# Kernel tuning notes

Hardware: AMD Instinct MI355X
Metric: run time of the kernel (lower is better)

## Reference

```python
import jax, jax.numpy as jnp
import numpy as np

B, L, N_KERNELS = 16, 4096, 512
KSS = [7, 9, 11]


def _make_params():
    """Replicates ROCKET.__init__ random kernel generation (numpy RNG, seed 0).

    Note: the torch code builds Conv1d with padding=2*padding (padding doubled),
    computes the padding from the *float* dilation, and casts dilation to int
    for the conv. We reproduce that exactly.
    """
    rng = np.random.default_rng(0)
    ks_a, d_a, pad_a, w_l, b_l = [], [], [], [], []
    for _ in range(N_KERNELS):
        ks = int(rng.choice(KSS))
        d_f = 2.0 ** rng.uniform(0.0, np.log2((L - 1) // (ks - 1)))
        d = int(d_f)
        p0 = int((ks - 1) * d_f // 2) if rng.integers(2) == 1 else 0
        pad = 2 * p0  # conv1d padding arg is 2*padding in the source
        w = rng.standard_normal(ks).astype(np.float32)
        w -= w.mean()  # weight -= weight.mean() (c_in=1 -> mean over ks)
        b = np.float32(2.0 * (rng.random() - 0.5))
        ks_a.append(ks); d_a.append(d); pad_a.append(pad)
        w_l.append(w); b_l.append(b)
    P = max(pad_a)  # global pad applied once to x; per-kernel offset corrects
    groups = {}
    order = []
    for ks in KSS:
        ids = [i for i in range(N_KERNELS) if ks_a[i] == ks]
        order += ids
        off = np.stack([[P - pad_a[i] + k * d_a[i] for k in range(ks)] for i in ids]).astype(np.int32)
        lout = np.array([L + 2 * pad_a[i] - d_a[i] * (ks - 1) for i in ids], np.int32)
        w = np.stack([w_l[i] for i in ids]).astype(np.float32)
        b = np.array([b_l[i] for i in ids], np.float32)
        groups[ks] = (w, b, off, lout)
    perm = np.argsort(np.array(order)).astype(np.int32)  # grouped -> original order
    return groups, perm, P


def setup_inputs() -> dict:
    key = jax.random.key(0)
    x = jax.random.normal(key, (B, 1, L), dtype=jnp.float32)
    groups, perm, P = _make_params()
    inp = {"x": x, "perm": jnp.asarray(perm), "P": int(P)}
    for gi, ks in enumerate(KSS):
        w, b, off, lout = groups[ks]
        inp[f"w{gi}"] = jnp.asarray(w)
        inp[f"b{gi}"] = jnp.asarray(b)
        inp[f"off{gi}"] = jnp.asarray(off)
        inp[f"lout{gi}"] = jnp.asarray(lout)
    return inp


def _group_feats(x_pad, w, b, off, lout, Lmax, Lp):
    # x_pad: [B, Lp]; w: [G, ks]; off: [G, ks]; lout: [G]
    t = jnp.arange(Lmax)
    out = b[None, :, None]  # [1, G, 1]
    ks = w.shape[-1]
    for k in range(ks):  # ks <= 11 taps of the dilated conv, batched over G kernels
        idx = jnp.clip(off[:, k][:, None] + t[None, :], 0, Lp - 1)  # [G, Lmax]
        out = out + w[:, k][None, :, None] * x_pad[:, idx]  # [B, G, Lmax]
    valid = (t[None, :] < lout[:, None])[None]  # [1, G, Lmax]
    mx = jnp.max(jnp.where(valid, out, jnp.finfo(out.dtype).min), axis=-1)  # [B, G]
    ppv = jnp.where(valid, out > 0, False).sum(-1).astype(out.dtype) / lout[None, :].astype(out.dtype)
    return mx, ppv


def reference(x, w0, b0, off0, lout0, w1, b1, off1, lout1, w2, b2, off2, lout2, perm, P):
    xs = x[:, 0, :]  # c_in = 1
    Lseq = xs.shape[-1]
    Lmax = 2 * Lseq + 16  # static bound: lout <= 2L + max(ks)
    Lp = Lseq + 2 * P
    x_pad = jnp.pad(xs, ((0, 0), (P, P)))
    mxs, ppvs = [], []
    for (w, b, off, lout) in ((w0, b0, off0, lout0), (w1, b1, off1, lout1), (w2, b2, off2, lout2)):
        mx, ppv = _group_feats(x_pad, w, b, off, lout, Lmax, Lp)
        mxs.append(mx)
        ppvs.append(ppv)
    mx = jnp.concatenate(mxs, axis=1)[:, perm]   # [B, n_kernels] original order
    ppv = jnp.concatenate(ppvs, axis=1)[:, perm]
    # torch.cat interleaves (max_i, ppv_i) along feature dim
    return jnp.stack([mx, ppv], axis=2).reshape(x.shape[0], -1)
```

## Files before the change

### kernel.cpp

```cpp
#include <hip/hip_runtime.h>
#include <math.h>

#define LSEQ 4096
#define NK 512
#define NB 16
#define NT 1024
#define CK 16
#define NCH (NK / CK)

typedef float v2f __attribute__((ext_vector_type(2)));

template <int KS>
__device__ __forceinline__ void rocket_body(
    const float* __restrict__ sx,
    const float* __restrict__ w, const float* __restrict__ bias,
    const int* __restrict__ off, const int* __restrict__ lout,
    int P, int li,
    float* smxc, int* scntc, int* sLoc)
{
    const int tid = threadIdx.x;

    float wk[KS];
#pragma unroll
    for (int k = 0; k < KS; ++k) wk[k] = w[li * KS + k];
    const int o0  = off[li * KS + 0];
    const int o1  = off[li * KS + 1];
    const int d   = o1 - o0;
    const int pad = P - o0;
    const float bi = bias[li];
    const int   Lo = lout[li];

    int t_lo = min(pad, Lo);
    int t_hi = min(Lo, LSEQ - (KS - 1) * d + pad);
    if (t_hi < t_lo) t_hi = t_lo;
    int T0 = (t_lo + 3) & ~3;
    int T1 = t_hi & ~3;
    if (T1 < T0) { T0 = 0; T1 = 0; }

    float mx  = -INFINITY;
    int   cnt = 0;

    for (int t = tid; t < T0; t += NT) {
        float y = bi;
        int idx = t - pad;
#pragma unroll
        for (int k = 0; k < KS; ++k) {
            int ic = min(max(idx, 0), LSEQ - 1);
            float xv = sx[ic];
            xv = ((unsigned)idx < (unsigned)LSEQ) ? xv : 0.0f;
            y = fmaf(wk[k], xv, y);
            idx += d;
        }
        mx = fmaxf(mx, y); cnt += (y > 0.0f);
    }

    int ebk[KS];
#pragma unroll
    for (int k = 0; k < KS; ++k) {
        const int A0 = T0 - pad + k * d;
        const int rk = A0 & 3;
        ebk[k] = rk * LSEQ + (k * d - pad - rk);
    }
    v2f mx2 = { -INFINITY, -INFINITY };
    for (int t = T0 + 4 * tid; t < T1; t += 4 * NT) {
        v2f y01 = { bi, bi }, y23 = { bi, bi };
#pragma unroll
        for (int kb = 0; kb < KS; kb += 4) {
            const int ke = (kb + 4 < KS) ? (kb + 4) : KS;
            float4 Xc[4];
#pragma unroll
            for (int k = kb; k < ke; ++k)
                Xc[k - kb] = *(const float4*)(sx + (t + ebk[k]));
#pragma unroll
            for (int k = kb; k < ke; ++k) {
                const v2f wv  = { wk[k], wk[k] };
                const v2f xlo = { Xc[k - kb].x, Xc[k - kb].y };
                const v2f xhi = { Xc[k - kb].z, Xc[k - kb].w };
                y01 = __builtin_elementwise_fma(wv, xlo, y01);
                y23 = __builtin_elementwise_fma(wv, xhi, y23);
            }
        }
        mx2 = __builtin_elementwise_max(mx2, __builtin_elementwise_max(y01, y23));
        cnt += (y01.x > 0.0f);
        cnt += (y01.y > 0.0f);
        cnt += (y23.x > 0.0f);
        cnt += (y23.y > 0.0f);
    }
    mx = fmaxf(mx, fmaxf(mx2.x, mx2.y));

    for (int t = T1 + tid; t < Lo; t += NT) {
        float y = bi;
        int idx = t - pad;
#pragma unroll
        for (int k = 0; k < KS; ++k) {
            int ic = min(max(idx, 0), LSEQ - 1);
            float xv = sx[ic];
            xv = ((unsigned)idx < (unsigned)LSEQ) ? xv : 0.0f;
            y = fmaf(wk[k], xv, y);
            idx += d;
        }
        mx = fmaxf(mx, y); cnt += (y > 0.0f);
    }

#pragma unroll
    for (int o = 32; o > 0; o >>= 1) {
        mx = fmaxf(mx, __shfl_down(mx, o, 64));
        cnt += __shfl_down(cnt, o, 64);
    }
    const int wid = tid >> 6;
    if ((tid & 63) == 0) { smxc[wid] = mx; scntc[wid] = cnt; }
    if (tid == 0) *sLoc = Lo;
}

__global__ __launch_bounds__(NT, 8) void rocket_v13_kernel(
    const float* __restrict__ x, const int* __restrict__ perm,
    const int* __restrict__ Pp,
    const float* __restrict__ w0, const float* __restrict__ b0,
    const int* __restrict__ off0, const int* __restrict__ l0,
    const float* __restrict__ w1, const float* __restrict__ b1,
    const int* __restrict__ off1, const int* __restrict__ l1,
    const float* __restrict__ w2, const float* __restrict__ b2,
    const int* __restrict__ off2, const int* __restrict__ l2,
    int n0, int n01,
    float* __restrict__ out)
{
    __shared__ float sx[4 * LSEQ];
    __shared__ int   sj[CK];
    __shared__ int   sLo[CK];
    __shared__ float smx[CK][16];
    __shared__ int   scnt[CK][16];

    const int chunk = blockIdx.x;
    const int b     = blockIdx.y;
    const int tid   = threadIdx.x;

    if (tid < NK) {
        const int p0 = perm[tid];
#pragma unroll
        for (int c = 0; c < CK; ++c) {
            if (p0 == chunk + NCH * c) sj[c] = tid;
        }
    }

    const float* xg = x + (size_t)b * LSEQ;
    const float4* x4 = (const float4*)xg;
    {
        const int m = tid;
        const float4 v = x4[m];
        const float4 n = x4[min(m + 1, LSEQ / 4 - 1)];
        const int e = 4 * m;
        *(float4*)(sx + e)            = v;
        *(float4*)(sx + LSEQ + e)     = make_float4(v.y, v.z, v.w, n.x);
        *(float4*)(sx + 2 * LSEQ + e) = make_float4(v.z, v.w, n.x, n.y);
        *(float4*)(sx + 3 * LSEQ + e) = make_float4(v.w, n.x, n.y, n.z);
    }
    __syncthreads();

    const int P = *Pp;

#pragma unroll 1
    for (int c = 0; c < CK; ++c) {
        const int gid = chunk + NCH * c;
        if (gid < n0) {
            rocket_body<7>(sx, w0, b0, off0, l0, P, gid, smx[c], scnt[c], &sLo[c]);
        } else if (gid < n01) {
            rocket_body<9>(sx, w1, b1, off1, l1, P, gid - n0, smx[c], scnt[c], &sLo[c]);
        } else {
            rocket_body<11>(sx, w2, b2, off2, l2, P, gid - n01, smx[c], scnt[c], &sLo[c]);
        }
    }
    __syncthreads();

    if (tid < CK) {
        const int c = tid;
        float m = smx[c][0];
        int   cn = scnt[c][0];
#pragma unroll
        for (int i = 1; i < 16; ++i) { m = fmaxf(m, smx[c][i]); cn += scnt[c][i]; }
        const int outj = sj[c];
        const int Lo   = sLo[c];
        out[b * (2 * NK) + 2 * outj]     = m;
        out[b * (2 * NK) + 2 * outj + 1] = (float)cn / (float)Lo;
    }
}

extern "C" void kernel_launch(void* const* d_in, const int* in_sizes, int n_in,
                              void* d_out, int out_size, void* d_ws, size_t ws_size,
                              hipStream_t stream) {
    const float* x    = (const float*)d_in[0];
    const int*   perm = (const int*)d_in[1];
    const int*   Pp   = (const int*)d_in[2];
    const float* w0   = (const float*)d_in[3];
    const float* b0   = (const float*)d_in[4];
    const int*   off0 = (const int*)d_in[5];
    const int*   l0   = (const int*)d_in[6];
    const float* w1   = (const float*)d_in[7];
    const float* b1   = (const float*)d_in[8];
    const int*   off1 = (const int*)d_in[9];
    const int*   l1   = (const int*)d_in[10];
    const float* w2   = (const float*)d_in[11];
    const float* b2   = (const float*)d_in[12];
    const int*   off2 = (const int*)d_in[13];
    const int*   l2   = (const int*)d_in[14];

    const int n0 = in_sizes[4];
    const int n1 = in_sizes[8];

    float* out = (float*)d_out;

    rocket_v13_kernel<<<dim3(NCH, NB), NT, 0, stream>>>(
        x, perm, Pp, w0, b0, off0, l0, w1, b1, off1, l1, w2, b2, off2, l2,
        n0, n0 + n1, out);
}
```

Measured before the change: 59.19 us.

## Assign one ROCKET kernel per wavefront instead of block-wide cooperation

Each of the 16 wavefronts in a block now computes one convolution kernel end to end and writes its max and PPV straight to global memory. Previously all 16 waves shared every kernel in the chunk and combined partials through shared memory. This drops the LDS partial arrays, the final __syncthreads and the per-kernel block-wide prologue and epilogue overhead. The cost is load imbalance: kernels in a block have different kernel sizes and output lengths, so the block lasts as long as its slowest wave.

```diff
diff --git a/kernel.cpp b/kernel.cpp
--- a/kernel.cpp
+++ b/kernel.cpp
@@ -11,14 +11,14 @@
 typedef float v2f __attribute__((ext_vector_type(2)));
 
 template <int KS>
-__device__ __forceinline__ void rocket_body(
+__device__ __forceinline__ void rocket_wave(
     const float* __restrict__ sx,
     const float* __restrict__ w, const float* __restrict__ bias,
     const int* __restrict__ off, const int* __restrict__ lout,
-    int P, int li,
-    float* smxc, int* scntc, int* sLoc)
+    int P, int li, int b, int outj,
+    float* __restrict__ out)
 {
-    const int tid = threadIdx.x;
+    const int lane = threadIdx.x & 63;
 
     float wk[KS];
 #pragma unroll
@@ -40,7 +40,7 @@
     float mx  = -INFINITY;
     int   cnt = 0;
 
-    for (int t = tid; t < T0; t += NT) {
+    for (int t = lane; t < T0; t += 64) {
         float y = bi;
         int idx = t - pad;
 #pragma unroll
@@ -62,7 +62,7 @@
         ebk[k] = rk * LSEQ + (k * d - pad - rk);
     }
     v2f mx2 = { -INFINITY, -INFINITY };
-    for (int t = T0 + 4 * tid; t < T1; t += 4 * NT) {
+    for (int t = T0 + 4 * lane; t < T1; t += 4 * 64) {
         v2f y01 = { bi, bi }, y23 = { bi, bi };
 #pragma unroll
         for (int kb = 0; kb < KS; kb += 4) {
@@ -88,7 +88,7 @@
     }
     mx = fmaxf(mx, fmaxf(mx2.x, mx2.y));
 
-    for (int t = T1 + tid; t < Lo; t += NT) {
+    for (int t = T1 + lane; t < Lo; t += 64) {
         float y = bi;
         int idx = t - pad;
 #pragma unroll
@@ -107,12 +107,13 @@
         mx = fmaxf(mx, __shfl_down(mx, o, 64));
         cnt += __shfl_down(cnt, o, 64);
     }
-    const int wid = tid >> 6;
-    if ((tid & 63) == 0) { smxc[wid] = mx; scntc[wid] = cnt; }
-    if (tid == 0) *sLoc = Lo;
+    if (lane == 0) {
+        out[b * (2 * NK) + 2 * outj]     = mx;
+        out[b * (2 * NK) + 2 * outj + 1] = (float)cnt / (float)Lo;
+    }
 }
 
-__global__ __launch_bounds__(NT, 8) void rocket_v13_kernel(
+__global__ __launch_bounds__(NT, 8) void rocket_v14_kernel(
     const float* __restrict__ x, const int* __restrict__ perm,
     const int* __restrict__ Pp,
     const float* __restrict__ w0, const float* __restrict__ b0,
@@ -126,9 +127,6 @@
 {
     __shared__ float sx[4 * LSEQ];
     __shared__ int   sj[CK];
-    __shared__ int   sLo[CK];
-    __shared__ float smx[CK][16];
-    __shared__ int   scnt[CK][16];
 
     const int chunk = blockIdx.x;
     const int b     = blockIdx.y;
@@ -158,29 +156,16 @@
 
     const int P = *Pp;
 
-#pragma unroll 1
-    for (int c = 0; c < CK; ++c) {
-        const int gid = chunk + NCH * c;
-        if (gid < n0) {
-            rocket_body<7>(sx, w0, b0, off0, l0, P, gid, smx[c], scnt[c], &sLo[c]);
-        } else if (gid < n01) {
-            rocket_body<9>(sx, w1, b1, off1, l1, P, gid - n0, smx[c], scnt[c], &sLo[c]);
-        } else {
-            rocket_body<11>(sx, w2, b2, off2, l2, P, gid - n01, smx[c], scnt[c], &sLo[c]);
-        }
-    }
-    __syncthreads();
+    const int wv  = tid >> 6;
+    const int gid = chunk + NCH * wv;
+    const int outj = sj[wv];
 
-    if (tid < CK) {
-        const int c = tid;
-        float m = smx[c][0];
-        int   cn = scnt[c][0];
-#pragma unroll
-        for (int i = 1; i < 16; ++i) { m = fmaxf(m, smx[c][i]); cn += scnt[c][i]; }
-        const int outj = sj[c];
-        const int Lo   = sLo[c];
-        out[b * (2 * NK) + 2 * outj]     = m;
-        out[b * (2 * NK) + 2 * outj + 1] = (float)cn / (float)Lo;
+    if (gid < n0) {
+        rocket_wave<7>(sx, w0, b0, off0, l0, P, gid, b, outj, out);
+    } else if (gid < n01) {
+        rocket_wave<9>(sx, w1, b1, off1, l1, P, gid - n0, b, outj, out);
+    } else {
+        rocket_wave<11>(sx, w2, b2, off2, l2, P, gid - n01, b, outj, out);
     }
 }
 
@@ -208,7 +193,7 @@
 
     float* out = (float*)d_out;
 
-    rocket_v13_kernel<<<dim3(NCH, NB), NT, 0, stream>>>(
+    rocket_v14_kernel<<<dim3(NCH, NB), NT, 0, stream>>>(
         x, perm, Pp, w0, b0, off0, l0, w1, b1, off1, l1, w2, b2, off2, l2,
         n0, n0 + n1, out);
 }
```

Result: slower. 63.57 us (+7.4%).
